# Optimization experiments

Hardware: AMD Instinct MI355X
Metric: run time of the kernel (lower is better)

The kernel has to match this reference:

```python
import jax, jax.numpy as jnp
import numpy as np

DIM = 2048
NUM_HEADS = 16
HEAD_DIM = DIM // NUM_HEADS  # 128


def setup_inputs() -> dict:
    key = jax.random.key(0)
    ks = jax.random.split(key, 5)
    scale = 0.02
    x = jax.random.normal(ks[0], (1, 2048, DIM), dtype=jnp.float32)
    # nn.Linear weights stored as [out_features, in_features]
    Wq = jax.random.normal(ks[1], (DIM, DIM), dtype=jnp.float32) * scale
    Wk = jax.random.normal(ks[2], (HEAD_DIM, DIM), dtype=jnp.float32) * scale
    Wv = jax.random.normal(ks[3], (HEAD_DIM, DIM), dtype=jnp.float32) * scale
    Wo = jax.random.normal(ks[4], (DIM, DIM), dtype=jnp.float32) * scale
    return {"x": x, "Wq": Wq, "Wk": Wk, "Wv": Wv, "Wo": Wo}


def reference(x, Wq, Wk, Wv, Wo):
    batch, seq_len, dim = x.shape
    q = x @ Wq.T                                   # [b, s, dim]
    k = x @ Wk.T                                   # [b, s, head_dim] (shared across heads)
    v = x @ Wv.T                                   # [b, s, head_dim]
    q = q.reshape(batch, seq_len, NUM_HEADS, HEAD_DIM).transpose(0, 2, 1, 3)  # [b, h, s, d]
    # MQA: single KV head broadcast across query heads (no materialized repeat)
    scores = jnp.einsum("bhqd,bkd->bhqk", q, k) / (HEAD_DIM ** 0.5)
    probs = jax.nn.softmax(scores, axis=-1)        # [b, h, q, k]
    out = jnp.einsum("bhqk,bkd->bhqd", probs, v)   # [b, h, s, d]
    out = out.transpose(0, 2, 1, 3).reshape(batch, seq_len, dim)
    return out @ Wo.T
```

## Files before the change

### kernel.cpp

```cpp
#include <hip/hip_runtime.h>
#include <cmath>

typedef float  float4_t __attribute__((ext_vector_type(4)));
typedef __bf16 bf16x8   __attribute__((ext_vector_type(8)));
typedef __bf16 bf16x4   __attribute__((ext_vector_type(4)));
typedef unsigned short u16;

__device__ __forceinline__ u16 f2bf(float f) {
    unsigned u = __float_as_uint(f);
    u += 0x7fffu + ((u >> 16) & 1u);
    return (u16)(u >> 16);
}

#define GLOAD_LDS16(g, l)                                              \
    __builtin_amdgcn_global_load_lds(                                  \
        (__attribute__((address_space(1))) void*)(g),                  \
        (__attribute__((address_space(3))) void*)(l), 16, 0, 0)

__global__ __launch_bounds__(256) void cast_all(const float* __restrict__ x,
                                                const float* __restrict__ wq,
                                                const float* __restrict__ wk,
                                                const float* __restrict__ wv,
                                                const float* __restrict__ wo,
                                                u16* __restrict__ xb, u16* __restrict__ wqb,
                                                u16* __restrict__ wkb, u16* __restrict__ wvb,
                                                u16* __restrict__ wob) {
    const int b = blockIdx.x;
    const float* src;
    u16* dst;
    int i;
    if (b < 4096)      { src = x;  dst = xb;  i = b * 256 + threadIdx.x; }
    else if (b < 8192) { src = wq; dst = wqb; i = (b - 4096) * 256 + threadIdx.x; }
    else if (b < 8448) { src = wk; dst = wkb; i = (b - 8192) * 256 + threadIdx.x; }
    else if (b < 8704) { src = wv; dst = wvb; i = (b - 8448) * 256 + threadIdx.x; }
    else               { src = wo; dst = wob; i = (b - 8704) * 256 + threadIdx.x; }
    float4 f = ((const float4*)src)[i];
    ushort4 r;
    r.x = f2bf(f.x); r.y = f2bf(f.y); r.z = f2bf(f.z); r.w = f2bf(f.w);
    ((ushort4*)dst)[i] = r;
}

template <typename EPI>
__device__ __forceinline__ void gemm128_core(const u16* __restrict__ A,
                                             const u16* __restrict__ B,
                                             int ldk, int klen, int bm, int bn, EPI epi) {
    __shared__ __align__(16) u16 As[128 * 32];
    __shared__ __align__(16) u16 Bs[128 * 32];
    const int tid  = threadIdx.x;
    const int lane = tid & 63, wave = tid >> 6;
    const int wm = wave >> 1, wn = wave & 1;
    const int quad = lane >> 4, l16 = lane & 15;

    float4_t acc[4][4] = {};
    const int r0 = tid >> 2;
    const int c0 = (tid & 3) * 8;

    for (int k0 = 0; k0 < klen; k0 += 32) {
#pragma unroll
        for (int i = 0; i < 2; ++i) {
            const int row = i * 64 + r0;
            const int e   = (i * 256 + tid) * 8;
            GLOAD_LDS16(A + (size_t)(bm + row) * ldk + k0 + c0, &As[e]);
            GLOAD_LDS16(B + (size_t)(bn + row) * ldk + k0 + c0, &Bs[e]);
        }
        __syncthreads();

        bf16x8 af[4], bfr[4];
#pragma unroll
        for (int mi = 0; mi < 4; ++mi)
            af[mi] = *(const bf16x8*)&As[(wm * 64 + mi * 16 + l16) * 32 + quad * 8];
#pragma unroll
        for (int ni = 0; ni < 4; ++ni)
            bfr[ni] = *(const bf16x8*)&Bs[(wn * 64 + ni * 16 + l16) * 32 + quad * 8];
#pragma unroll
        for (int mi = 0; mi < 4; ++mi)
#pragma unroll
            for (int ni = 0; ni < 4; ++ni)
                acc[mi][ni] = __builtin_amdgcn_mfma_f32_16x16x32_bf16(
                    af[mi], bfr[ni], acc[mi][ni], 0, 0, 0);
        __syncthreads();
    }

#pragma unroll
    for (int mi = 0; mi < 4; ++mi) {
        const int row = bm + wm * 64 + mi * 16 + quad * 4;
#pragma unroll
        for (int ni = 0; ni < 4; ++ni) {
            const int col = bn + wn * 64 + ni * 16 + l16;
#pragma unroll
            for (int r = 0; r < 4; ++r) epi(row + r, col, acc[mi][ni][r]);
        }
    }
}

__global__ __launch_bounds__(256) void gemm_qkv(const u16* __restrict__ A,
                                                const u16* __restrict__ B,
                                                u16* __restrict__ qb,
                                                u16* __restrict__ kb,
                                                u16* __restrict__ vtb) {
    gemm128_core(A, B, 2048, 2048, blockIdx.x * 128, blockIdx.y * 128,
                 [=](int row, int col, float v) {
                     if (col < 2048)
                         qb[(size_t)row * 2048 + col] = f2bf(v * 0.1275174313451427f);
                     else if (col < 2176)
                         kb[(size_t)row * 128 + (col - 2048)] = f2bf(v);
                     else
                         vtb[(size_t)(col - 2176) * 2048 + row] = f2bf(v);
                 });
}

__global__ __launch_bounds__(256) void gemm_out_s(const u16* __restrict__ A,
                                                  const u16* __restrict__ B,
                                                  float* __restrict__ P0,
                                                  float* __restrict__ P1) {
    const int z = blockIdx.z;
    float* __restrict__ P = z ? P1 : P0;
    gemm128_core(A + z * 1024, B + z * 1024, 2048, 1024,
                 blockIdx.x * 128, blockIdx.y * 128,
                 [=](int row, int col, float v) {
                     P[(size_t)row * 2048 + col] = v;
                 });
}

__global__ __launch_bounds__(256) void out_combine(const float* __restrict__ P0,
                                                   const float* __restrict__ P1,
                                                   float* __restrict__ out) {
    const int f = blockIdx.x * 256 + threadIdx.x;
    const float4 a = ((const float4*)P0)[f];
    const float4 b = ((const float4*)P1)[f];
    float4 r;
    r.x = a.x + b.x; r.y = a.y + b.y; r.z = a.z + b.z; r.w = a.w + b.w;
    ((float4*)out)[f] = r;
}

__global__ __launch_bounds__(256) void mqa_attn(const u16* __restrict__ Q,
                                                const u16* __restrict__ Kmat,
                                                const u16* __restrict__ Vt,
                                                float* __restrict__ Oacc0,
                                                float* __restrict__ Oacc1,
                                                float* __restrict__ Lsum) {
    __shared__ __align__(16) u16 Ks[4 * 32 * 32];
    __shared__ __align__(16) u16 Vts[128 * 32];
    __shared__ __align__(16) u16 Ps[4][32 * 36];
    const int tid  = threadIdx.x;
    const int wave = tid >> 6, lane = tid & 63;
    const int quad = lane >> 4, l16 = lane & 15;
    const int h     = blockIdx.y;
    const int ks    = blockIdx.z;
    const int qbase = blockIdx.x * 128 + wave * 32;
    const int kbase = ks * 1024;

    bf16x8 qf[2][4];
#pragma unroll
    for (int mt = 0; mt < 2; ++mt)
#pragma unroll
        for (int kb4 = 0; kb4 < 4; ++kb4)
            qf[mt][kb4] = *(const bf16x8*)(Q + (size_t)(qbase + mt * 16 + l16) * 2048 +
                                           h * 128 + kb4 * 32 + quad * 8);

    float4_t acc[2][8];
#pragma unroll
    for (int mt = 0; mt < 2; ++mt)
#pragma unroll
        for (int nt = 0; nt < 8; ++nt) acc[mt][nt] = (float4_t){0.f, 0.f, 0.f, 0.f};
    float lsum[8] = {};

    u16* pb = Ps[wave];

    for (int s = 0; s < 32; ++s) {
        const int k0 = kbase + s * 32;
#pragma unroll
        for (int i = 0; i < 2; ++i) {
            const int slot = i * 256 + tid;
            const int kb4 = slot >> 7, win = slot & 127;
            const int row = win >> 2, ch = (win & 3) * 8;
            GLOAD_LDS16(Kmat + (size_t)(k0 + row) * 128 + kb4 * 32 + ch, &Ks[slot * 8]);
        }
#pragma unroll
        for (int i = 0; i < 2; ++i) {
            const int slot = i * 256 + tid;
            const int d = slot >> 2, ch = (slot & 3) * 8;
            GLOAD_LDS16(Vt + (size_t)d * 2048 + k0 + ch, &Vts[slot * 8]);
        }
        __syncthreads();

#pragma unroll
        for (int ct = 0; ct < 2; ++ct) {
            float4_t s0 = (float4_t){0.f, 0.f, 0.f, 0.f};
            float4_t s1 = (float4_t){0.f, 0.f, 0.f, 0.f};
#pragma unroll
            for (int kb4 = 0; kb4 < 4; ++kb4) {
                bf16x8 kf = *(const bf16x8*)&Ks[kb4 * 1024 + (ct * 16 + l16) * 32 + quad * 8];
                s0 = __builtin_amdgcn_mfma_f32_16x16x32_bf16(qf[0][kb4], kf, s0, 0, 0, 0);
                s1 = __builtin_amdgcn_mfma_f32_16x16x32_bf16(qf[1][kb4], kf, s1, 0, 0, 0);
            }
#pragma unroll
            for (int r = 0; r < 4; ++r) {
                const float e0 = exp2f(s0[r]);
                const float e1 = exp2f(s1[r]);
                lsum[r]     += e0;
                lsum[4 + r] += e1;
                pb[(quad * 4 + r) * 36 + ct * 16 + l16]      = f2bf(e0);
                pb[(16 + quad * 4 + r) * 36 + ct * 16 + l16] = f2bf(e1);
            }
        }
        bf16x8 pa[2];
#pragma unroll
        for (int mt = 0; mt < 2; ++mt) {
            const int base = (mt * 16 + l16) * 36 + quad * 8;
            bf16x4 lo = *(const bf16x4*)&pb[base];
            bf16x4 hi = *(const bf16x4*)&pb[base + 4];
            pa[mt] = __builtin_shufflevector(lo, hi, 0, 1, 2, 3, 4, 5, 6, 7);
        }
#pragma unroll
        for (int nt = 0; nt < 8; ++nt) {
            bf16x8 vf = *(const bf16x8*)&Vts[(nt * 16 + l16) * 32 + quad * 8];
            acc[0][nt] = __builtin_amdgcn_mfma_f32_16x16x32_bf16(pa[0], vf, acc[0][nt], 0, 0, 0);
            acc[1][nt] = __builtin_amdgcn_mfma_f32_16x16x32_bf16(pa[1], vf, acc[1][nt], 0, 0, 0);
        }
        __syncthreads();
    }

    float* __restrict__ Op = ks ? Oacc1 : Oacc0;
#pragma unroll
    for (int mt = 0; mt < 2; ++mt)
#pragma unroll
        for (int r = 0; r < 4; ++r) {
            const int row = qbase + mt * 16 + quad * 4 + r;
            const size_t base = ((size_t)h * 2048 + row) * 128;
            float lrow = lsum[mt * 4 + r];
#pragma unroll
            for (int off = 1; off < 16; off <<= 1) lrow += __shfl_xor(lrow, off);
            if (l16 == 0) Lsum[(size_t)ks * 32768 + h * 2048 + row] = lrow;
#pragma unroll
            for (int nt = 0; nt < 8; ++nt)
                Op[base + nt * 16 + l16] = acc[mt][nt][r];
        }
}

__global__ __launch_bounds__(256) void attn_combine(const float* __restrict__ O0,
                                                    const float* __restrict__ O1,
                                                    const float* __restrict__ L,
                                                    u16* __restrict__ attn) {
    const int f = blockIdx.x * 256 + threadIdx.x;
    const int d4 = f & 31, h = (f >> 5) & 15, q = f >> 9;
    const int li = h * 2048 + q;
    const float inv = 1.0f / (L[li] + L[32768 + li]);
    const int oi = li * 32 + d4;
    const float4 a = ((const float4*)O0)[oi];
    const float4 b = ((const float4*)O1)[oi];
    ushort4 r;
    r.x = f2bf((a.x + b.x) * inv);
    r.y = f2bf((a.y + b.y) * inv);
    r.z = f2bf((a.z + b.z) * inv);
    r.w = f2bf((a.w + b.w) * inv);
    ((ushort4*)attn)[f] = r;
}

extern "C" void kernel_launch(void* const* d_in, const int* in_sizes, int n_in,
                              void* d_out, int out_size, void* d_ws, size_t ws_size,
                              hipStream_t stream) {
    const float* x  = (const float*)d_in[0];
    const float* Wq = (const float*)d_in[1];
    const float* Wk = (const float*)d_in[2];
    const float* Wv = (const float*)d_in[3];
    const float* Wo = (const float*)d_in[4];
    float* out = (float*)d_out;

    u16* ws   = (u16*)d_ws;
    u16* xb   = ws;
    u16* Wqb  = xb  + (4 << 20);
    u16* Wkb  = Wqb + (4 << 20);
    u16* Wvb  = Wkb + (256 << 10);
    u16* Wob  = Wvb + (256 << 10);
    u16* qb   = Wob + (4 << 20);
    u16* kb   = qb  + (4 << 20);
    u16* vtb  = kb  + (256 << 10);
    u16* attn = vtb + (256 << 10);
    float* Oacc0 = (float*)ws;
    float* Oacc1 = (float*)(attn + (4 << 20));
    float* Lsum  = Oacc1 + (4 << 20);
    float* Po0   = (float*)ws;
    float* Po1   = Oacc1;

    cast_all<<<12800, 256, 0, stream>>>(x, Wq, Wk, Wv, Wo, xb, Wqb, Wkb, Wvb, Wob);

    gemm_qkv<<<dim3(16, 18), 256, 0, stream>>>(xb, Wqb, qb, kb, vtb);
    mqa_attn<<<dim3(16, 16, 2), 256, 0, stream>>>(qb, kb, vtb, Oacc0, Oacc1, Lsum);
    attn_combine<<<4096, 256, 0, stream>>>(Oacc0, Oacc1, Lsum, attn);
    gemm_out_s<<<dim3(16, 16, 2), 256, 0, stream>>>(attn, Wob, Po0, Po1);
    out_combine<<<4096, 256, 0, stream>>>(Po0, Po1, out);
}
```

Before: 254.9 us.

## Split-K the QKV GEMM and widen attention/out-proj splits to three

The QKV projection is now split over K into two halves. One half writes bf16 directly and the other writes fp32 partials that a new combine kernel adds in and scales. The attention KV range and the output projection K dimension are split three ways (704/672/672), with the output buffer reused as one partial. The goal is to fill more CUs, since the previous grids (288 and 512 blocks) underused a 256-CU GPU. The cost is extra partial traffic, an extra combine kernel, and a bf16 round-trip on half of the QKV sum, which loses some precision.

```diff
diff --git a/kernel.cpp b/kernel.cpp
--- a/kernel.cpp
+++ b/kernel.cpp
@@ -10,6 +10,9 @@
     unsigned u = __float_as_uint(f);
     u += 0x7fffu + ((u >> 16) & 1u);
     return (u16)(u >> 16);
+}
+__device__ __forceinline__ float bf2f(u16 h) {
+    return __uint_as_float((unsigned)h << 16);
 }
 
 #define GLOAD_LDS16(g, l)                                              \
@@ -93,51 +96,101 @@
     }
 }
 
-__global__ __launch_bounds__(256) void gemm_qkv(const u16* __restrict__ A,
-                                                const u16* __restrict__ B,
-                                                u16* __restrict__ qb,
-                                                u16* __restrict__ kb,
-                                                u16* __restrict__ vtb) {
-    gemm128_core(A, B, 2048, 2048, blockIdx.x * 128, blockIdx.y * 128,
+__global__ __launch_bounds__(256) void gemm_qkv_s(const u16* __restrict__ A,
+                                                  const u16* __restrict__ B,
+                                                  u16* __restrict__ qb,
+                                                  u16* __restrict__ kb,
+                                                  u16* __restrict__ vtb,
+                                                  float* __restrict__ Pq) {
+    const int z = blockIdx.z;
+    gemm128_core(A + z * 1024, B + z * 1024, 2048, 1024,
+                 blockIdx.x * 128, blockIdx.y * 128,
                  [=](int row, int col, float v) {
-                     if (col < 2048)
-                         qb[(size_t)row * 2048 + col] = f2bf(v * 0.1275174313451427f);
-                     else if (col < 2176)
-                         kb[(size_t)row * 128 + (col - 2048)] = f2bf(v);
-                     else
-                         vtb[(size_t)(col - 2176) * 2048 + row] = f2bf(v);
+                     if (z == 0) {
+                         if (col < 2048)
+                             qb[(size_t)row * 2048 + col] = f2bf(v);
+                         else if (col < 2176)
+                             kb[(size_t)row * 128 + (col - 2048)] = f2bf(v);
+                         else
+                             vtb[(size_t)(col - 2176) * 2048 + row] = f2bf(v);
+                     } else {
+                         Pq[(size_t)row * 2304 + col] = v;
+                     }
                  });
+}
+
+__global__ __launch_bounds__(256) void qkv_combine(const float* __restrict__ P,
+                                                   u16* __restrict__ qb,
+                                                   u16* __restrict__ kb,
+                                                   u16* __restrict__ vtb) {
+    const int f = blockIdx.x * 256 + threadIdx.x;
+    const int r = f / 576, c = f - r * 576;
+    const int col = c * 4;
+    const float4 p = ((const float4*)P)[f];
+    if (col < 2048) {
+        const float s = 0.1275174313451427f;
+        ushort4 d = ((ushort4*)qb)[(r * 2048 + col) >> 2];
+        ushort4 o;
+        o.x = f2bf((bf2f(d.x) + p.x) * s);
+        o.y = f2bf((bf2f(d.y) + p.y) * s);
+        o.z = f2bf((bf2f(d.z) + p.z) * s);
+        o.w = f2bf((bf2f(d.w) + p.w) * s);
+        ((ushort4*)qb)[(r * 2048 + col) >> 2] = o;
+    } else if (col < 2176) {
+        const int c2 = col - 2048;
+        ushort4 d = ((ushort4*)kb)[(r * 128 + c2) >> 2];
+        ushort4 o;
+        o.x = f2bf(bf2f(d.x) + p.x);
+        o.y = f2bf(bf2f(d.y) + p.y);
+        o.z = f2bf(bf2f(d.z) + p.z);
+        o.w = f2bf(bf2f(d.w) + p.w);
+        ((ushort4*)kb)[(r * 128 + c2) >> 2] = o;
+    } else {
+        const int c2 = col - 2176;
+        const float pv[4] = {p.x, p.y, p.z, p.w};
+#pragma unroll
+        for (int j = 0; j < 4; ++j) {
+            const size_t idx = (size_t)(c2 + j) * 2048 + r;
+            vtb[idx] = f2bf(bf2f(vtb[idx]) + pv[j]);
+        }
+    }
 }
 
 __global__ __launch_bounds__(256) void gemm_out_s(const u16* __restrict__ A,
                                                   const u16* __restrict__ B,
                                                   float* __restrict__ P0,
-                                                  float* __restrict__ P1) {
+                                                  float* __restrict__ P1,
+                                                  float* __restrict__ P2) {
     const int z = blockIdx.z;
-    float* __restrict__ P = z ? P1 : P0;
-    gemm128_core(A + z * 1024, B + z * 1024, 2048, 1024,
+    const int koff = (z == 0) ? 0 : 704 + 672 * (z - 1);
+    const int klen = (z == 0) ? 704 : 672;
+    float* __restrict__ P = (z == 0) ? P0 : (z == 1 ? P1 : P2);
+    gemm128_core(A + koff, B + koff, 2048, klen,
                  blockIdx.x * 128, blockIdx.y * 128,
                  [=](int row, int col, float v) {
                      P[(size_t)row * 2048 + col] = v;
                  });
 }
 
-__global__ __launch_bounds__(256) void out_combine(const float* __restrict__ P0,
-                                                   const float* __restrict__ P1,
+__global__ __launch_bounds__(256) void out_combine(const float* __restrict__ P1,
+                                                   const float* __restrict__ P2,
                                                    float* __restrict__ out) {
     const int f = blockIdx.x * 256 + threadIdx.x;
-    const float4 a = ((const float4*)P0)[f];
-    const float4 b = ((const float4*)P1)[f];
+    const float4 o = ((const float4*)out)[f];
+    const float4 a = ((const float4*)P1)[f];
+    const float4 b = ((const float4*)P2)[f];
     float4 r;
-    r.x = a.x + b.x; r.y = a.y + b.y; r.z = a.z + b.z; r.w = a.w + b.w;
+    r.x = o.x + a.x + b.x; r.y = o.y + a.y + b.y;
+    r.z = o.z + a.z + b.z; r.w = o.w + a.w + b.w;
     ((float4*)out)[f] = r;
 }
 
 __global__ __launch_bounds__(256) void mqa_attn(const u16* __restrict__ Q,
                                                 const u16* __restrict__ Kmat,
                                                 const u16* __restrict__ Vt,
-                                                float* __restrict__ Oacc0,
-                                                float* __restrict__ Oacc1,
+                                                float* __restrict__ A0,
+                                                float* __restrict__ A1,
+                                                float* __restrict__ A2,
                                                 float* __restrict__ Lsum) {
     __shared__ __align__(16) u16 Ks[4 * 32 * 32];
     __shared__ __align__(16) u16 Vts[128 * 32];
@@ -146,9 +199,10 @@
     const int wave = tid >> 6, lane = tid & 63;
     const int quad = lane >> 4, l16 = lane & 15;
     const int h     = blockIdx.y;
-    const int ks    = blockIdx.z;
+    const int kz    = blockIdx.z;
     const int qbase = blockIdx.x * 128 + wave * 32;
-    const int kbase = ks * 1024;
+    const int koff  = (kz == 0) ? 0 : 704 + 672 * (kz - 1);
+    const int nst   = (kz == 0) ? 22 : 21;
 
     bf16x8 qf[2][4];
 #pragma unroll
@@ -167,8 +221,8 @@
 
     u16* pb = Ps[wave];
 
-    for (int s = 0; s < 32; ++s) {
-        const int k0 = kbase + s * 32;
+    for (int s = 0; s < nst; ++s) {
+        const int k0 = koff + s * 32;
 #pragma unroll
         for (int i = 0; i < 2; ++i) {
             const int slot = i * 256 + tid;
@@ -221,7 +275,7 @@
         __syncthreads();
     }
 
-    float* __restrict__ Op = ks ? Oacc1 : Oacc0;
+    float* __restrict__ Op = (kz == 0) ? A0 : (kz == 1 ? A1 : A2);
 #pragma unroll
     for (int mt = 0; mt < 2; ++mt)
 #pragma unroll
@@ -231,29 +285,31 @@
             float lrow = lsum[mt * 4 + r];
 #pragma unroll
             for (int off = 1; off < 16; off <<= 1) lrow += __shfl_xor(lrow, off);
-            if (l16 == 0) Lsum[(size_t)ks * 32768 + h * 2048 + row] = lrow;
+            if (l16 == 0) Lsum[(size_t)kz * 32768 + h * 2048 + row] = lrow;
 #pragma unroll
             for (int nt = 0; nt < 8; ++nt)
                 Op[base + nt * 16 + l16] = acc[mt][nt][r];
         }
 }
 
-__global__ __launch_bounds__(256) void attn_combine(const float* __restrict__ O0,
-                                                    const float* __restrict__ O1,
+__global__ __launch_bounds__(256) void attn_combine(const float* __restrict__ A0,
+                                                    const float* __restrict__ A1,
+                                                    const float* __restrict__ A2,
                                                     const float* __restrict__ L,
                                                     u16* __restrict__ attn) {
     const int f = blockIdx.x * 256 + threadIdx.x;
     const int d4 = f & 31, h = (f >> 5) & 15, q = f >> 9;
     const int li = h * 2048 + q;
-    const float inv = 1.0f / (L[li] + L[32768 + li]);
+    const float inv = 1.0f / (L[li] + L[32768 + li] + L[65536 + li]);
     const int oi = li * 32 + d4;
-    const float4 a = ((const float4*)O0)[oi];
-    const float4 b = ((const float4*)O1)[oi];
+    const float4 a = ((const float4*)A0)[oi];
+    const float4 b = ((const float4*)A1)[oi];
+    const float4 c = ((const float4*)A2)[oi];
     ushort4 r;
-    r.x = f2bf((a.x + b.x) * inv);
-    r.y = f2bf((a.y + b.y) * inv);
-    r.z = f2bf((a.z + b.z) * inv);
-    r.w = f2bf((a.w + b.w) * inv);
+    r.x = f2bf((a.x + b.x + c.x) * inv);
+    r.y = f2bf((a.y + b.y + c.y) * inv);
+    r.z = f2bf((a.z + b.z + c.z) * inv);
+    r.w = f2bf((a.w + b.w + c.w) * inv);
     ((ushort4*)attn)[f] = r;
 }
 
@@ -277,17 +333,20 @@
     u16* kb   = qb  + (4 << 20);
     u16* vtb  = kb  + (256 << 10);
     u16* attn = vtb + (256 << 10);
-    float* Oacc0 = (float*)ws;
-    float* Oacc1 = (float*)(attn + (4 << 20));
-    float* Lsum  = Oacc1 + (4 << 20);
-    float* Po0   = (float*)ws;
-    float* Po1   = Oacc1;
+    float* Pq = (float*)(attn + (4 << 20));
+    float* Ab0 = (float*)ws;
+    float* Ab1 = Pq;
+    float* Ab2 = out;
+    float* Lsum = Ab1 + (4 << 20);
+    float* Po1 = Ab0;
+    float* Po2 = Ab1;
 
     cast_all<<<12800, 256, 0, stream>>>(x, Wq, Wk, Wv, Wo, xb, Wqb, Wkb, Wvb, Wob);
 
-    gemm_qkv<<<dim3(16, 18), 256, 0, stream>>>(xb, Wqb, qb, kb, vtb);
-    mqa_attn<<<dim3(16, 16, 2), 256, 0, stream>>>(qb, kb, vtb, Oacc0, Oacc1, Lsum);
-    attn_combine<<<4096, 256, 0, stream>>>(Oacc0, Oacc1, Lsum, attn);
-    gemm_out_s<<<dim3(16, 16, 2), 256, 0, stream>>>(attn, Wob, Po0, Po1);
-    out_combine<<<4096, 256, 0, stream>>>(Po0, Po1, out);
-}
+    gemm_qkv_s<<<dim3(16, 18, 2), 256, 0, stream>>>(xb, Wqb, qb, kb, vtb, Pq);
+    qkv_combine<<<4608, 256, 0, stream>>>(Pq, qb, kb, vtb);
+    mqa_attn<<<dim3(16, 16, 3), 256, 0, stream>>>(qb, kb, vtb, Ab0, Ab1, Ab2, Lsum);
+    attn_combine<<<4096, 256, 0, stream>>>(Ab0, Ab1, Ab2, Lsum, attn);
+    gemm_out_s<<<dim3(16, 16, 3), 256, 0, stream>>>(attn, Wob, out, Po1, Po2);
+    out_combine<<<4096, 256, 0, stream>>>(Po1, Po2, out);
+}
```

New measurement: 277.9 us. +9.1%, slower.
